# Kernel optimization log

Measured on AMD Instinct MI355X. Metric: run time of the kernel, lower is better.

The kernel has to match this reference:

```python
import jax, jax.numpy as jnp
import numpy as np

B, T, D, H, F = 2, 2048, 2048, 16, 8192
DH = D // H  # 128
EPS = 1e-6   # flax LayerNorm default


def _layernorm(x, scale, bias):
    mu = jnp.mean(x, axis=-1, keepdims=True)
    var = jnp.mean(jnp.square(x - mu), axis=-1, keepdims=True)
    return (x - mu) * jax.lax.rsqrt(var + EPS) * scale + bias


def setup_inputs() -> dict:
    key = jax.random.key(0)
    ks = jax.random.split(key, 8)
    w = 0.02
    return {
        "x": jax.random.normal(ks[0], (B, T, D), jnp.float32),
        "ln1_scale": jnp.ones((D,), jnp.float32),
        "ln1_bias": jnp.zeros((D,), jnp.float32),
        "w_qkv": jax.random.normal(ks[1], (D, 3 * D), jnp.float32) * w,
        "b_qkv": jnp.zeros((3 * D,), jnp.float32),
        "ln2_scale": jnp.ones((D,), jnp.float32),
        "ln2_bias": jnp.zeros((D,), jnp.float32),
        "w1": jax.random.normal(ks[2], (D, F), jnp.float32) * w,
        "b1": jnp.zeros((F,), jnp.float32),
        "w2": jax.random.normal(ks[3], (F, D), jnp.float32) * w,
        "b2": jnp.zeros((D,), jnp.float32),
    }


def reference(x, ln1_scale, ln1_bias, w_qkv, b_qkv, ln2_scale, ln2_bias, w1, b1, w2, b2):
    # --- pre-LN causal self-attention (training=False -> dropout = identity) ---
    r = _layernorm(x, ln1_scale, ln1_bias)
    qkv = r @ w_qkv + b_qkv                       # [B,T,3D]
    q, k, v = jnp.split(qkv, 3, axis=-1)
    q = q.reshape(B, T, H, DH)
    k = k.reshape(B, T, H, DH)
    v = v.reshape(B, T, H, DH)
    attn = jnp.einsum('bthd,bThd->bhtT', q, k) / jnp.sqrt(jnp.float32(DH))
    causal = jnp.tril(jnp.ones((T, T), bool))
    attn = jnp.where(causal, attn, -jnp.inf)
    attn = jax.nn.softmax(attn, axis=-1)
    out = jnp.einsum('bhtT,bThd->bthd', attn, v).reshape(B, T, D)
    # NOTE: original module has no output projection after attention.
    x = x + out
    # --- MLP block ---
    r = _layernorm(x, ln2_scale, ln2_bias)
    h = jax.nn.gelu(r @ w1 + b1, approximate=True)  # flax nn.gelu default
    x = x + (h @ w2 + b2)
    return x
```

## Files before the change

### kernel.cpp

```cpp
#include <hip/hip_runtime.h>
#include <hip/hip_bf16.h>
#include <stdint.h>
#include <stddef.h>

using bf16_t = __hip_bfloat16;
typedef __attribute__((ext_vector_type(8))) short short8;
typedef __attribute__((ext_vector_type(4))) float f32x4;

__device__ __forceinline__ void gload_lds16(const void* g, void* l) {
  __builtin_amdgcn_global_load_lds((const __attribute__((address_space(1))) void*)g,
                                   (__attribute__((address_space(3))) void*)l,
                                   16, 0, 0);
}

__global__ __launch_bounds__(256) void k_transpose_cvt(const float* __restrict__ in,
                                                       bf16_t* __restrict__ out,
                                                       int K, int N) {
  __shared__ float tile[64][65];
  int n0 = blockIdx.x * 64, k0 = blockIdx.y * 64;
  int t = threadIdx.x;
#pragma unroll
  for (int i = 0; i < 16; ++i) {
    int idx = t + i * 256;
    int kk = idx >> 6, nn = idx & 63;
    tile[kk][nn] = in[(size_t)(k0 + kk) * N + n0 + nn];
  }
  __syncthreads();
#pragma unroll
  for (int i = 0; i < 16; ++i) {
    int idx = t + i * 256;
    int nn = idx >> 6, kk = idx & 63;
    out[(size_t)(n0 + nn) * K + k0 + kk] = __float2bfloat16(tile[kk][nn]);
  }
}

__global__ __launch_bounds__(256) void k_layernorm(const float* __restrict__ x,
                                                   const float* __restrict__ gam,
                                                   const float* __restrict__ bet,
                                                   bf16_t* __restrict__ out) {
  int row = blockIdx.x, t = threadIdx.x;
  const float4* xr = (const float4*)(x + (size_t)row * 2048);
  float4 a = xr[t], b = xr[t + 256];
  float s  = a.x + a.y + a.z + a.w + b.x + b.y + b.z + b.w;
  float s2 = a.x*a.x + a.y*a.y + a.z*a.z + a.w*a.w
           + b.x*b.x + b.y*b.y + b.z*b.z + b.w*b.w;
#pragma unroll
  for (int off = 32; off >= 1; off >>= 1) {
    s  += __shfl_xor(s, off);
    s2 += __shfl_xor(s2, off);
  }
  __shared__ float red[8];
  if ((t & 63) == 0) { red[t >> 6] = s; red[4 + (t >> 6)] = s2; }
  __syncthreads();
  float S  = red[0] + red[1] + red[2] + red[3];
  float S2 = red[4] + red[5] + red[6] + red[7];
  float mu = S * (1.0f / 2048.0f);
  float var = S2 * (1.0f / 2048.0f) - mu * mu;
  float rstd = rsqrtf(var + 1e-6f);
  const float4* gv = (const float4*)gam;
  const float4* bv = (const float4*)bet;
  float4 g1 = gv[t], g2 = gv[t + 256], c1 = bv[t], c2 = bv[t + 256];
  bf16_t* orow = out + (size_t)row * 2048;
  orow[4*t + 0]    = __float2bfloat16((a.x - mu) * rstd * g1.x + c1.x);
  orow[4*t + 1]    = __float2bfloat16((a.y - mu) * rstd * g1.y + c1.y);
  orow[4*t + 2]    = __float2bfloat16((a.z - mu) * rstd * g1.z + c1.z);
  orow[4*t + 3]    = __float2bfloat16((a.w - mu) * rstd * g1.w + c1.w);
  orow[1024 + 4*t + 0] = __float2bfloat16((b.x - mu) * rstd * g2.x + c2.x);
  orow[1024 + 4*t + 1] = __float2bfloat16((b.y - mu) * rstd * g2.y + c2.y);
  orow[1024 + 4*t + 2] = __float2bfloat16((b.z - mu) * rstd * g2.z + c2.z);
  orow[1024 + 4*t + 3] = __float2bfloat16((b.w - mu) * rstd * g2.w + c2.w);
}

template <int EPI>
__global__ __launch_bounds__(256, 2) void k_gemm4(const bf16_t* __restrict__ A,
                                                  const bf16_t* __restrict__ Bt,
                                                  const float* __restrict__ bias,
                                                  bf16_t* __restrict__ Cb,
                                                  float* __restrict__ Cf,
                                                  int Ndim, int LDA, int LDB,
                                                  int Kdim, int nkch) {
  __shared__ __align__(16) char lds[65536];
  int nwg = gridDim.x;
  int orig = blockIdx.x;
  int wg = (orig & 7) * (nwg >> 3) + (orig >> 3);
  int bpc = nwg / nkch;
  int chunk = wg / bpc;
  int rem = wg - chunk * bpc;
  int m0 = (rem & 15) * 256;
  int n0 = (rem >> 4) * 128;
  int tid = threadIdx.x;
  int w = tid >> 6, lane = tid & 63;
  int lr = lane & 15, lk = lane >> 4;
  int wr = w >> 1, wc = w & 1;

  int srow = tid >> 2;
  int scol = ((tid & 3) ^ ((tid >> 3) & 3)) << 3;
  const bf16_t* Ag = A + (size_t)m0 * LDA + (size_t)chunk * Kdim;
  const bf16_t* Bg = Bt + (size_t)n0 * LDB + (size_t)chunk * Kdim;
  const bf16_t* pA0 = Ag + (size_t)(srow)       * LDA + scol;
  const bf16_t* pA1 = Ag + (size_t)(srow + 64)  * LDA + scol;
  const bf16_t* pA2 = Ag + (size_t)(srow + 128) * LDA + scol;
  const bf16_t* pA3 = Ag + (size_t)(srow + 192) * LDA + scol;
  const bf16_t* pB0 = Bg + (size_t)(srow)       * LDB + scol;
  const bf16_t* pB1 = Bg + (size_t)(srow + 64)  * LDB + scol;
  int dst = tid * 16;

  int ch = (lk ^ ((lr >> 1) & 3)) * 16;
  int aoff[8], boff[4];
#pragma unroll
  for (int mf = 0; mf < 8; ++mf) aoff[mf] = (wr * 128 + mf * 16 + lr) * 64 + ch;
#pragma unroll
  for (int nf = 0; nf < 4; ++nf) boff[nf] = 49152 + (wc * 64 + nf * 16 + lr) * 64 + ch;

  f32x4 acc[8][4];
#pragma unroll
  for (int i = 0; i < 8; ++i)
#pragma unroll
    for (int j = 0; j < 4; ++j) acc[i][j] = (f32x4){0.f, 0.f, 0.f, 0.f};
  short8 af[8], bq[4];

#define STAGE_A()  do { \
    gload_lds16(pA0, lds + a_wr + dst);          \
    gload_lds16(pA1, lds + a_wr + 4096 + dst);   \
    gload_lds16(pA2, lds + a_wr + 8192 + dst);   \
    gload_lds16(pA3, lds + a_wr + 12288 + dst);  \
    pA0 += 32; pA1 += 32; pA2 += 32; pA3 += 32; } while (0)
#define STAGE_B()  do { \
    gload_lds16(pB0, lds + 49152 + b_wr + dst);        \
    gload_lds16(pB1, lds + 49152 + b_wr + 4096 + dst); \
    pB0 += 32; pB1 += 32; } while (0)
#define READ_FR()  do { \
    _Pragma("unroll") for (int mf = 0; mf < 8; ++mf) \
      af[mf] = *(const short8*)(lds + a_rd + aoff[mf]); \
    _Pragma("unroll") for (int nf = 0; nf < 4; ++nf) \
      bq[nf] = *(const short8*)(lds + b_rd + boff[nf]); } while (0)
#define MMAC()  do { \
    _Pragma("unroll") for (int mf = 0; mf < 8; ++mf) \
      _Pragma("unroll") for (int nf = 0; nf < 4; ++nf) \
        acc[mf][nf] = __builtin_amdgcn_mfma_f32_16x16x32_bf16(af[mf], bq[nf], acc[mf][nf], 0, 0, 0); } while (0)
#define LGKM0()  do { asm volatile("s_waitcnt lgkmcnt(0)" ::: "memory"); __builtin_amdgcn_sched_barrier(0); } while (0)
#define VM(N)    asm volatile("s_waitcnt vmcnt(%0)" :: "i"(N) : "memory")
#define BARRIER() asm volatile("s_barrier" ::: "memory")

  int a_rd = 0, a_wr = 32768;
  int b_rd = 0, b_wr = 8192;
  const int NT = Kdim >> 5;

  { int sva = a_wr, svb = b_wr;
    a_wr = 0;     STAGE_A();
    b_wr = 0;     STAGE_B();
    a_wr = 16384; STAGE_A();
    a_wr = sva;   b_wr = svb; }
  VM(4);
  BARRIER();

  for (int t = 0; t < NT - 2; ++t) {
    STAGE_B();
    STAGE_A();
    READ_FR();
    LGKM0();
    __builtin_amdgcn_s_setprio(1);
    MMAC();
    __builtin_amdgcn_s_setprio(0);
    VM(4);
    BARRIER();
    int fr = a_rd; a_rd = (a_rd == 32768) ? 0 : a_rd + 16384; a_wr = fr;
    fr = b_rd; b_rd = b_wr; b_wr = fr;
  }
  {
    STAGE_B();
    READ_FR();
    LGKM0();
    __builtin_amdgcn_s_setprio(1);
    MMAC();
    __builtin_amdgcn_s_setprio(0);
    VM(0);
    BARRIER();
    a_rd = (a_rd == 32768) ? 0 : a_rd + 16384;
    b_rd = b_wr;
  }
  {
    READ_FR();
    LGKM0();
    MMAC();
  }
#undef STAGE_A
#undef STAGE_B
#undef READ_FR
#undef MMAC
#undef LGKM0
#undef VM
#undef BARRIER

#pragma unroll
  for (int mf = 0; mf < 8; ++mf) {
#pragma unroll
    for (int nf = 0; nf < 4; ++nf) {
#pragma unroll
      for (int r = 0; r < 4; ++r) {
        int rw = m0 + wr * 128 + mf * 16 + lk * 4 + r;
        int cl = n0 + wc * 64 + nf * 16 + lr;
        float v = acc[mf][nf][r];
        size_t gi = (size_t)rw * Ndim + cl;
        if (EPI == 0) {
          Cb[gi] = __float2bfloat16(v + bias[cl]);
        } else if (EPI == 1) {
          float vv = v + bias[cl];
          float u = vv * (vv * vv * 0.044715f + 1.0f) * 0.7978845608028654f;
          float gl = 0.5f * vv * (1.0f + tanhf(u));
          Cb[gi] = __float2bfloat16(gl);
        } else {
          Cf[(size_t)chunk * 4096 * Ndim + gi] = v;
        }
      }
    }
  }
}

__global__ __launch_bounds__(256) void k_reduce(const float* __restrict__ P,
                                                const float* __restrict__ b2,
                                                float* __restrict__ out) {
  int i = blockIdx.x * 1024 + threadIdx.x * 4;
  float4 p0 = *(const float4*)(P + i);
  float4 p1 = *(const float4*)(P + 8388608 + i);
  float4 bb = *(const float4*)(b2 + (i & 2047));
  float4 o  = *(float4*)(out + i);
  o.x += bb.x + p0.x + p1.x;
  o.y += bb.y + p0.y + p1.y;
  o.z += bb.z + p0.z + p1.z;
  o.w += bb.w + p0.w + p1.w;
  *(float4*)(out + i) = o;
}

__global__ __launch_bounds__(256) void k_transpose_v(const bf16_t* __restrict__ qkv,
                                                     bf16_t* __restrict__ vT) {
  __shared__ bf16_t tile[64][72];
  int bid = blockIdx.x;
  int tt = bid & 31;
  int dt = (bid >> 5) & 1;
  int h  = (bid >> 6) & 15;
  int b  = bid >> 10;
  int t0 = tt * 64, d0 = dt * 64;
  int t = threadIdx.x;
  const bf16_t* src = qkv + (size_t)(b * 2048) * 6144 + 4096 + h * 128;
#pragma unroll
  for (int i = 0; i < 16; ++i) {
    int idx = t + i * 256;
    int rr = idx >> 6, cc = idx & 63;
    tile[rr][cc] = src[(size_t)(t0 + rr) * 6144 + d0 + cc];
  }
  __syncthreads();
  bf16_t* dst = vT + (size_t)(b * 16 + h) * 128 * 2048;
#pragma unroll
  for (int i = 0; i < 16; ++i) {
    int idx = t + i * 256;
    int rr = idx >> 6, cc = idx & 63;
    dst[(size_t)(d0 + rr) * 2048 + t0 + cc] = tile[cc][rr];
  }
}

__global__ __launch_bounds__(256, 2) void k_attn(const bf16_t* __restrict__ qkv,
                                                 const bf16_t* __restrict__ vT,
                                                 const float* __restrict__ x,
                                                 float* __restrict__ out) {
  __shared__ __align__(16) bf16_t Pl[4][32][40];
  int j = blockIdx.x;
  int bh = j & 31;
  int cq = j >> 5;
  int b = bh >> 4, h = bh & 15;
  int w = threadIdx.x >> 6, lane = threadIdx.x & 63;
  int lr = lane & 15, lk = lane >> 4;
  int c = (w == 0) ? cq : (w == 1) ? (63 - cq) : (w == 2) ? (31 - cq) : (32 + cq);
  int q0 = c * 32;
  const bf16_t* qb = qkv + (size_t)(b * 2048) * 6144 + h * 128;
  const bf16_t* kb = qb + 2048;
  const bf16_t* vb = vT + (size_t)(b * 16 + h) * 128 * 2048;
  short8 qf[2][4];
#pragma unroll
  for (int qg = 0; qg < 2; ++qg)
#pragma unroll
    for (int d4 = 0; d4 < 4; ++d4)
      qf[qg][d4] = *(const short8*)(qb + (size_t)(q0 + qg * 16 + lr) * 6144 + d4 * 32 + lk * 8);
  float m[2][4], l[2][4];
#pragma unroll
  for (int qg = 0; qg < 2; ++qg)
#pragma unroll
    for (int r = 0; r < 4; ++r) { m[qg][r] = -1e30f; l[qg][r] = 0.f; }
  f32x4 o[2][8] = {};
  int nkt = c + 1;
  const float sc = 0.08838834764831845f;
  for (int kt = 0; kt < nkt; ++kt) {
    int tk0 = kt * 32;
    short8 vf[8];
#pragma unroll
    for (int d8 = 0; d8 < 8; ++d8)
      vf[d8] = *(const short8*)(vb + (size_t)(d8 * 16 + lr) * 2048 + tk0 + lk * 8);
    short8 kf[2][4];
#pragma unroll
    for (int nt = 0; nt < 2; ++nt)
#pragma unroll
      for (int d4 = 0; d4 < 4; ++d4)
        kf[nt][d4] = *(const short8*)(kb + (size_t)(tk0 + nt * 16 + lr) * 6144 + d4 * 32 + lk * 8);
    f32x4 s[2][2] = {};
#pragma unroll
    for (int d4 = 0; d4 < 4; ++d4)
#pragma unroll
      for (int qg = 0; qg < 2; ++qg)
#pragma unroll
        for (int nt = 0; nt < 2; ++nt)
          s[qg][nt] = __builtin_amdgcn_mfma_f32_16x16x32_bf16(qf[qg][d4], kf[nt][d4], s[qg][nt], 0, 0, 0);
#pragma unroll
    for (int qg = 0; qg < 2; ++qg) {
      float sv[2][4], mt[4];
#pragma unroll
      for (int r = 0; r < 4; ++r) {
        int qr = q0 + qg * 16 + lk * 4 + r;
#pragma unroll
        for (int nt = 0; nt < 2; ++nt) {
          float v = s[qg][nt][r] * sc;
          int kc = tk0 + nt * 16 + lr;
          sv[nt][r] = (kc > qr) ? -1e30f : v;
        }
        mt[r] = fmaxf(sv[0][r], sv[1][r]);
      }
#pragma unroll
      for (int off = 1; off < 16; off <<= 1)
#pragma unroll
        for (int r = 0; r < 4; ++r) mt[r] = fmaxf(mt[r], __shfl_xor(mt[r], off));
      float alpha[4], rs[4];
#pragma unroll
      for (int r = 0; r < 4; ++r) {
        float mn = fmaxf(m[qg][r], mt[r]);
        alpha[r] = __expf(m[qg][r] - mn);
        m[qg][r] = mn;
      }
#pragma unroll
      for (int r = 0; r < 4; ++r) {
        float p0 = __expf(sv[0][r] - m[qg][r]);
        float p1 = __expf(sv[1][r] - m[qg][r]);
        rs[r] = p0 + p1;
        Pl[w][qg * 16 + lk * 4 + r][lr]      = __float2bfloat16(p0);
        Pl[w][qg * 16 + lk * 4 + r][16 + lr] = __float2bfloat16(p1);
      }
#pragma unroll
      for (int off = 1; off < 16; off <<= 1)
#pragma unroll
        for (int r = 0; r < 4; ++r) rs[r] += __shfl_xor(rs[r], off);
#pragma unroll
      for (int r = 0; r < 4; ++r) l[qg][r] = l[qg][r] * alpha[r] + rs[r];
#pragma unroll
      for (int d8 = 0; d8 < 8; ++d8)
#pragma unroll
        for (int r = 0; r < 4; ++r) o[qg][d8][r] *= alpha[r];
    }
    asm volatile("s_waitcnt lgkmcnt(0)" ::: "memory");
    short8 pf[2];
#pragma unroll
    for (int qg = 0; qg < 2; ++qg)
      pf[qg] = *(const short8*)(&Pl[w][qg * 16 + lr][lk * 8]);
#pragma unroll
    for (int d8 = 0; d8 < 8; ++d8)
#pragma unroll
      for (int qg = 0; qg < 2; ++qg)
        o[qg][d8] = __builtin_amdgcn_mfma_f32_16x16x32_bf16(pf[qg], vf[d8], o[qg][d8], 0, 0, 0);
  }
#pragma unroll
  for (int qg = 0; qg < 2; ++qg)
#pragma unroll
    for (int d8 = 0; d8 < 8; ++d8)
#pragma unroll
      for (int r = 0; r < 4; ++r) {
        int qr = q0 + qg * 16 + lk * 4 + r;
        int cl = h * 128 + d8 * 16 + lr;
        size_t gi = (size_t)(b * 2048 + qr) * 2048 + cl;
        out[gi] = x[gi] + o[qg][d8][r] / l[qg][r];
      }
}

extern "C" void kernel_launch(void* const* d_in, const int* in_sizes, int n_in,
                              void* d_out, int out_size, void* d_ws, size_t ws_size,
                              hipStream_t stream) {
  const float* x    = (const float*)d_in[0];
  const float* ln1s = (const float*)d_in[1];
  const float* ln1b = (const float*)d_in[2];
  const float* wqkv = (const float*)d_in[3];
  const float* bqkv = (const float*)d_in[4];
  const float* ln2s = (const float*)d_in[5];
  const float* ln2b = (const float*)d_in[6];
  const float* w1   = (const float*)d_in[7];
  const float* b1   = (const float*)d_in[8];
  const float* w2   = (const float*)d_in[9];
  const float* b2   = (const float*)d_in[10];
  float* out = (float*)d_out;
  char* ws = (char*)d_ws;

  bf16_t* r     = (bf16_t*)(ws + 0);
  bf16_t* vT    = (bf16_t*)(ws + 0);
  float*  part  = (float*)(ws + 0);
  bf16_t* qkv   = (bf16_t*)(ws + 16777216);
  bf16_t* w1T   = (bf16_t*)(ws + 67108864);
  bf16_t* w2T   = (bf16_t*)(ws + 100663296);
  bf16_t* h     = (bf16_t*)(ws + 134217728);
  bf16_t* wqkvT = (bf16_t*)(ws + 134217728);

  k_transpose_cvt<<<dim3(96, 32),  256, 0, stream>>>(wqkv, wqkvT, 2048, 6144);
  k_transpose_cvt<<<dim3(128, 32), 256, 0, stream>>>(w1,   w1T,   2048, 8192);
  k_transpose_cvt<<<dim3(32, 128), 256, 0, stream>>>(w2,   w2T,   8192, 2048);
  k_layernorm<<<4096, 256, 0, stream>>>(x, ln1s, ln1b, r);
  k_gemm4<0><<<768, 256, 0, stream>>>(r, wqkvT, bqkv, qkv, nullptr, 6144, 2048, 2048, 2048, 1);
  k_transpose_v<<<2048, 256, 0, stream>>>(qkv, vT);
  k_attn<<<512, 256, 0, stream>>>(qkv, vT, x, out);
  k_layernorm<<<4096, 256, 0, stream>>>(out, ln2s, ln2b, r);
  k_gemm4<1><<<1024, 256, 0, stream>>>(r, w1T, b1, h, nullptr, 8192, 2048, 2048, 2048, 1);
  k_gemm4<3><<<512, 256, 0, stream>>>(h, w2T, nullptr, nullptr, part, 2048, 8192, 8192, 4096, 2);
  k_reduce<<<8192, 256, 0, stream>>>(part, b2, out);
}
```

Baseline: 685.3 us.

## Widen GEMM tile to 256x256, fuse split-K reduce via atomics, cheaper GELU

The GEMM tile grows from 256x128 to 256x256, which doubles the B staging and LDS to 96KB and runs one workgroup per CU with 8x8 accumulator fragments per wave. This raises arithmetic intensity and halves the grid. The separate split-K reduction kernel is dropped: the second MLP GEMM adds its partial sums and bias directly into the output with float atomics. The GELU tanh is rewritten using __expf. The larger register footprint may spill or lower occupancy, the atomics make the summation order nondeterministic, and the exp-based tanh can overflow for large inputs.

```diff
diff --git a/kernel.cpp b/kernel.cpp
--- a/kernel.cpp
+++ b/kernel.cpp
@@ -72,14 +72,14 @@
 }
 
 template <int EPI>
-__global__ __launch_bounds__(256, 2) void k_gemm4(const bf16_t* __restrict__ A,
+__global__ __launch_bounds__(256, 1) void k_gemm5(const bf16_t* __restrict__ A,
                                                   const bf16_t* __restrict__ Bt,
                                                   const float* __restrict__ bias,
                                                   bf16_t* __restrict__ Cb,
                                                   float* __restrict__ Cf,
                                                   int Ndim, int LDA, int LDB,
                                                   int Kdim, int nkch) {
-  __shared__ __align__(16) char lds[65536];
+  __shared__ __align__(16) char lds[98304];
   int nwg = gridDim.x;
   int orig = blockIdx.x;
   int wg = (orig & 7) * (nwg >> 3) + (orig >> 3);
@@ -87,7 +87,7 @@
   int chunk = wg / bpc;
   int rem = wg - chunk * bpc;
   int m0 = (rem & 15) * 256;
-  int n0 = (rem >> 4) * 128;
+  int n0 = (rem >> 4) * 256;
   int tid = threadIdx.x;
   int w = tid >> 6, lane = tid & 63;
   int lr = lane & 15, lk = lane >> 4;
@@ -103,89 +103,83 @@
   const bf16_t* pA3 = Ag + (size_t)(srow + 192) * LDA + scol;
   const bf16_t* pB0 = Bg + (size_t)(srow)       * LDB + scol;
   const bf16_t* pB1 = Bg + (size_t)(srow + 64)  * LDB + scol;
+  const bf16_t* pB2 = Bg + (size_t)(srow + 128) * LDB + scol;
+  const bf16_t* pB3 = Bg + (size_t)(srow + 192) * LDB + scol;
   int dst = tid * 16;
 
   int ch = (lk ^ ((lr >> 1) & 3)) * 16;
-  int aoff[8], boff[4];
+  int aoff[8], boff[8];
 #pragma unroll
   for (int mf = 0; mf < 8; ++mf) aoff[mf] = (wr * 128 + mf * 16 + lr) * 64 + ch;
 #pragma unroll
-  for (int nf = 0; nf < 4; ++nf) boff[nf] = 49152 + (wc * 64 + nf * 16 + lr) * 64 + ch;
-
-  f32x4 acc[8][4];
+  for (int nf = 0; nf < 8; ++nf) boff[nf] = 49152 + (wc * 128 + nf * 16 + lr) * 64 + ch;
+
+  f32x4 acc[8][8];
 #pragma unroll
   for (int i = 0; i < 8; ++i)
 #pragma unroll
-    for (int j = 0; j < 4; ++j) acc[i][j] = (f32x4){0.f, 0.f, 0.f, 0.f};
-  short8 af[8], bq[4];
-
-#define STAGE_A()  do { \
-    gload_lds16(pA0, lds + a_wr + dst);          \
-    gload_lds16(pA1, lds + a_wr + 4096 + dst);   \
-    gload_lds16(pA2, lds + a_wr + 8192 + dst);   \
-    gload_lds16(pA3, lds + a_wr + 12288 + dst);  \
-    pA0 += 32; pA1 += 32; pA2 += 32; pA3 += 32; } while (0)
-#define STAGE_B()  do { \
-    gload_lds16(pB0, lds + 49152 + b_wr + dst);        \
-    gload_lds16(pB1, lds + 49152 + b_wr + 4096 + dst); \
-    pB0 += 32; pB1 += 32; } while (0)
-#define READ_FR()  do { \
+    for (int j = 0; j < 8; ++j) acc[i][j] = (f32x4){0.f, 0.f, 0.f, 0.f};
+  short8 af[8], bq[8];
+
+#define STAGE(base) do { \
+    gload_lds16(pA0, lds + (base) + dst);                 \
+    gload_lds16(pA1, lds + (base) + 4096 + dst);          \
+    gload_lds16(pA2, lds + (base) + 8192 + dst);          \
+    gload_lds16(pA3, lds + (base) + 12288 + dst);         \
+    gload_lds16(pB0, lds + 49152 + (base) + dst);         \
+    gload_lds16(pB1, lds + 49152 + (base) + 4096 + dst);  \
+    gload_lds16(pB2, lds + 49152 + (base) + 8192 + dst);  \
+    gload_lds16(pB3, lds + 49152 + (base) + 12288 + dst); \
+    pA0 += 32; pA1 += 32; pA2 += 32; pA3 += 32;           \
+    pB0 += 32; pB1 += 32; pB2 += 32; pB3 += 32; } while (0)
+#define READ_FR(base) do { \
     _Pragma("unroll") for (int mf = 0; mf < 8; ++mf) \
-      af[mf] = *(const short8*)(lds + a_rd + aoff[mf]); \
-    _Pragma("unroll") for (int nf = 0; nf < 4; ++nf) \
-      bq[nf] = *(const short8*)(lds + b_rd + boff[nf]); } while (0)
-#define MMAC()  do { \
+      af[mf] = *(const short8*)(lds + (base) + aoff[mf]); \
+    _Pragma("unroll") for (int nf = 0; nf < 8; ++nf) \
+      bq[nf] = *(const short8*)(lds + (base) + boff[nf]); } while (0)
+#define MMAC() do { \
     _Pragma("unroll") for (int mf = 0; mf < 8; ++mf) \
-      _Pragma("unroll") for (int nf = 0; nf < 4; ++nf) \
+      _Pragma("unroll") for (int nf = 0; nf < 8; ++nf) \
         acc[mf][nf] = __builtin_amdgcn_mfma_f32_16x16x32_bf16(af[mf], bq[nf], acc[mf][nf], 0, 0, 0); } while (0)
 #define LGKM0()  do { asm volatile("s_waitcnt lgkmcnt(0)" ::: "memory"); __builtin_amdgcn_sched_barrier(0); } while (0)
 #define VM(N)    asm volatile("s_waitcnt vmcnt(%0)" :: "i"(N) : "memory")
 #define BARRIER() asm volatile("s_barrier" ::: "memory")
 
-  int a_rd = 0, a_wr = 32768;
-  int b_rd = 0, b_wr = 8192;
   const int NT = Kdim >> 5;
-
-  { int sva = a_wr, svb = b_wr;
-    a_wr = 0;     STAGE_A();
-    b_wr = 0;     STAGE_B();
-    a_wr = 16384; STAGE_A();
-    a_wr = sva;   b_wr = svb; }
-  VM(4);
+  int rdb = 0, wrb = 32768;
+
+  STAGE(0);
+  STAGE(16384);
+  VM(8);
   BARRIER();
 
   for (int t = 0; t < NT - 2; ++t) {
-    STAGE_B();
-    STAGE_A();
-    READ_FR();
+    STAGE(wrb);
+    READ_FR(rdb);
     LGKM0();
     __builtin_amdgcn_s_setprio(1);
     MMAC();
     __builtin_amdgcn_s_setprio(0);
-    VM(4);
+    VM(8);
     BARRIER();
-    int fr = a_rd; a_rd = (a_rd == 32768) ? 0 : a_rd + 16384; a_wr = fr;
-    fr = b_rd; b_rd = b_wr; b_wr = fr;
+    int old = rdb; rdb = (rdb == 32768) ? 0 : rdb + 16384; wrb = old;
   }
   {
-    STAGE_B();
-    READ_FR();
+    READ_FR(rdb);
     LGKM0();
     __builtin_amdgcn_s_setprio(1);
     MMAC();
     __builtin_amdgcn_s_setprio(0);
     VM(0);
     BARRIER();
-    a_rd = (a_rd == 32768) ? 0 : a_rd + 16384;
-    b_rd = b_wr;
+    rdb = (rdb == 32768) ? 0 : rdb + 16384;
   }
   {
-    READ_FR();
+    READ_FR(rdb);
     LGKM0();
     MMAC();
   }
-#undef STAGE_A
-#undef STAGE_B
+#undef STAGE
 #undef READ_FR
 #undef MMAC
 #undef LGKM0
@@ -195,41 +189,28 @@
 #pragma unroll
   for (int mf = 0; mf < 8; ++mf) {
 #pragma unroll
-    for (int nf = 0; nf < 4; ++nf) {
+    for (int nf = 0; nf < 8; ++nf) {
 #pragma unroll
       for (int r = 0; r < 4; ++r) {
         int rw = m0 + wr * 128 + mf * 16 + lk * 4 + r;
-        int cl = n0 + wc * 64 + nf * 16 + lr;
+        int cl = n0 + wc * 128 + nf * 16 + lr;
         float v = acc[mf][nf][r];
         size_t gi = (size_t)rw * Ndim + cl;
         if (EPI == 0) {
           Cb[gi] = __float2bfloat16(v + bias[cl]);
         } else if (EPI == 1) {
           float vv = v + bias[cl];
-          float u = vv * (vv * vv * 0.044715f + 1.0f) * 0.7978845608028654f;
-          float gl = 0.5f * vv * (1.0f + tanhf(u));
-          Cb[gi] = __float2bfloat16(gl);
+          float u = vv * (vv * vv * 0.044715f + 1.0f) * 1.5957691216057308f;
+          float e = __expf(u);
+          float th = (e - 1.0f) / (e + 1.0f);
+          Cb[gi] = __float2bfloat16(0.5f * vv * (1.0f + th));
         } else {
-          Cf[(size_t)chunk * 4096 * Ndim + gi] = v;
+          float add = v + (chunk == 0 ? bias[cl] : 0.0f);
+          atomicAdd(&Cf[gi], add);
         }
       }
     }
   }
-}
-
-__global__ __launch_bounds__(256) void k_reduce(const float* __restrict__ P,
-                                                const float* __restrict__ b2,
-                                                float* __restrict__ out) {
-  int i = blockIdx.x * 1024 + threadIdx.x * 4;
-  float4 p0 = *(const float4*)(P + i);
-  float4 p1 = *(const float4*)(P + 8388608 + i);
-  float4 bb = *(const float4*)(b2 + (i & 2047));
-  float4 o  = *(float4*)(out + i);
-  o.x += bb.x + p0.x + p1.x;
-  o.y += bb.y + p0.y + p1.y;
-  o.z += bb.z + p0.z + p1.z;
-  o.w += bb.w + p0.w + p1.w;
-  *(float4*)(out + i) = o;
 }
 
 __global__ __launch_bounds__(256) void k_transpose_v(const bf16_t* __restrict__ qkv,
@@ -396,7 +377,6 @@
 
   bf16_t* r     = (bf16_t*)(ws + 0);
   bf16_t* vT    = (bf16_t*)(ws + 0);
-  float*  part  = (float*)(ws + 0);
   bf16_t* qkv   = (bf16_t*)(ws + 16777216);
   bf16_t* w1T   = (bf16_t*)(ws + 67108864);
   bf16_t* w2T   = (bf16_t*)(ws + 100663296);
@@ -407,11 +387,10 @@
   k_transpose_cvt<<<dim3(128, 32), 256, 0, stream>>>(w1,   w1T,   2048, 8192);
   k_transpose_cvt<<<dim3(32, 128), 256, 0, stream>>>(w2,   w2T,   8192, 2048);
   k_layernorm<<<4096, 256, 0, stream>>>(x, ln1s, ln1b, r);
-  k_gemm4<0><<<768, 256, 0, stream>>>(r, wqkvT, bqkv, qkv, nullptr, 6144, 2048, 2048, 2048, 1);
+  k_gemm5<0><<<384, 256, 0, stream>>>(r, wqkvT, bqkv, qkv, nullptr, 6144, 2048, 2048, 2048, 1);
   k_transpose_v<<<2048, 256, 0, stream>>>(qkv, vT);
   k_attn<<<512, 256, 0, stream>>>(qkv, vT, x, out);
   k_layernorm<<<4096, 256, 0, stream>>>(out, ln2s, ln2b, r);
-  k_gemm4<1><<<1024, 256, 0, stream>>>(r, w1T, b1, h, nullptr, 8192, 2048, 2048, 2048, 1);
-  k_gemm4<3><<<512, 256, 0, stream>>>(h, w2T, nullptr, nullptr, part, 2048, 8192, 8192, 4096, 2);
-  k_reduce<<<8192, 256, 0, stream>>>(part, b2, out);
-}
+  k_gemm5<1><<<512, 256, 0, stream>>>(r, w1T, b1, h, nullptr, 8192, 2048, 2048, 2048, 1);
+  k_gemm5<3><<<256, 256, 0, stream>>>(h, w2T, b2, nullptr, out, 2048, 8192, 8192, 4096, 2);
+}
```

After: 785.4 us. +14.6%, slower.
